# Performance work log

Measured on AMD Instinct MI355X. Metric: run time of the kernel, lower is better.

The kernel has to match this reference:

```python
import math
import jax, jax.numpy as jnp
import numpy as np

D, L, E, O, Q, H, DH, T, B, N, FF = 1024, 8, 768, 1024, 16, 16, 64, 320, 64, 577, 4096
EPS = 1e-5


def layernorm(x, g, b):
    m = jnp.mean(x, axis=-1, keepdims=True)
    v = jnp.var(x, axis=-1, keepdims=True)
    return (x - m) * jax.lax.rsqrt(v + EPS) * g + b


def timestep_sinusoid(t):
    # diffusers Timesteps(320, flip_sin_to_cos=True, freq_shift=0)
    half = T // 2
    freqs = jnp.exp(-math.log(10000.0) * jnp.arange(half, dtype=jnp.float32) / half)
    args = t.astype(jnp.float32)[:, None] * freqs[None, :]
    return jnp.concatenate([jnp.cos(args), jnp.sin(args)], axis=-1)  # flipped order


def setup_inputs() -> dict:
    key = jax.random.key(0)
    ks = iter(jax.random.split(key, 32))
    std = 0.02
    inp = {}
    inp["x"] = jax.random.normal(next(ks), (B, N, E), jnp.float32)
    inp["timestep"] = jax.random.randint(next(ks), (B,), 0, 1000, jnp.int64 if jax.config.jax_enable_x64 else jnp.int32)
    inp["latents"] = jax.random.normal(next(ks), (1, Q, D), jnp.float32) / math.sqrt(D)
    inp["proj_in_w"] = jax.random.normal(next(ks), (D, E), jnp.float32) * std
    inp["proj_in_b"] = jnp.zeros((D,), jnp.float32)
    inp["time_w1"] = jax.random.normal(next(ks), (D, T), jnp.float32) * std
    inp["time_b1"] = jnp.zeros((D,), jnp.float32)
    inp["time_w2"] = jax.random.normal(next(ks), (D, D), jnp.float32) * std
    inp["time_b2"] = jnp.zeros((D,), jnp.float32)
    inp["ln1_g"] = jnp.ones((L, D), jnp.float32)
    inp["ln1_b"] = jnp.zeros((L, D), jnp.float32)
    inp["ln2_g"] = jnp.ones((L, D), jnp.float32)
    inp["ln2_b"] = jnp.zeros((L, D), jnp.float32)
    inp["q_w"] = jax.random.normal(next(ks), (L, D, D), jnp.float32) * std
    inp["kv_w"] = jax.random.normal(next(ks), (L, 2 * D, D), jnp.float32) * std
    inp["out_w"] = jax.random.normal(next(ks), (L, D, D), jnp.float32) * std
    inp["ffln_g"] = jnp.ones((L, D), jnp.float32)
    inp["ffln_b"] = jnp.zeros((L, D), jnp.float32)
    inp["ff_w1"] = jax.random.normal(next(ks), (L, FF, D), jnp.float32) * std
    inp["ff_w2"] = jax.random.normal(next(ks), (L, D, FF), jnp.float32) * std
    inp["ada_w"] = jax.random.normal(next(ks), (L, 4 * D, D), jnp.float32) * std
    inp["ada_b"] = jnp.zeros((L, 4 * D), jnp.float32)
    inp["proj_out_w"] = jax.random.normal(next(ks), (O, D), jnp.float32) * std
    inp["proj_out_b"] = jnp.zeros((O,), jnp.float32)
    inp["nout_g"] = jnp.ones((O,), jnp.float32)
    inp["nout_b"] = jnp.zeros((O,), jnp.float32)
    return inp


def reference(x, timestep, latents, proj_in_w, proj_in_b, time_w1, time_b1, time_w2, time_b2,
              ln1_g, ln1_b, ln2_g, ln2_b, q_w, kv_w, out_w, ffln_g, ffln_b, ff_w1, ff_w2,
              ada_w, ada_b, proj_out_w, proj_out_b, nout_g, nout_b):
    b = x.shape[0]
    # timestep embedding
    t_emb = timestep_sinusoid(timestep).astype(x.dtype)
    temb = jax.nn.silu(t_emb @ time_w1.T + time_b1) @ time_w2.T + time_b2  # [B, D]

    lat = jnp.broadcast_to(latents, (b, Q, D))
    xp = x @ proj_in_w.T + proj_in_b + temb[:, None, :]  # [B, N, D]

    sc = 1.0 / math.sqrt(math.sqrt(DH))
    for i in range(L):
        mod = jax.nn.silu(temb) @ ada_w[i].T + ada_b[i]  # [B, 4D]
        shift_msa, scale_msa, shift_mlp, scale_mlp = jnp.split(mod, 4, axis=-1)

        # PerceiverAttention with AdaLN-modulated latents
        xn = layernorm(xp, ln1_g[i], ln1_b[i])
        lt = layernorm(lat, ln2_g[i], ln2_b[i])
        lt = lt * (1.0 + scale_msa[:, None, :]) + shift_msa[:, None, :]
        q = (lt @ q_w[i].T).reshape(b, Q, H, DH).transpose(0, 2, 1, 3)       # [B,H,Q,DH]
        kv_in = jnp.concatenate([xn, lt], axis=1)                             # [B,N+Q,D]
        kv = kv_in @ kv_w[i].T
        k, v = jnp.split(kv, 2, axis=-1)
        kl = kv_in.shape[1]
        k = k.reshape(b, kl, H, DH).transpose(0, 2, 1, 3)
        v = v.reshape(b, kl, H, DH).transpose(0, 2, 1, 3)
        w = jnp.einsum('bhqd,bhkd->bhqk', q * sc, k * sc)
        w = jax.nn.softmax(w.astype(jnp.float32), axis=-1).astype(q.dtype)
        o = jnp.einsum('bhqk,bhkd->bhqd', w, v).transpose(0, 2, 1, 3).reshape(b, Q, H * DH)
        lat = o @ out_w[i].T + lat

        # FFN with AdaLN modulation after its LayerNorm
        h = layernorm(lat, ffln_g[i], ffln_b[i])
        h = h * (1.0 + scale_mlp[:, None, :]) + shift_mlp[:, None, :]
        h = jax.nn.gelu(h @ ff_w1[i].T, approximate=False)
        lat = h @ ff_w2[i].T + lat

    out = lat @ proj_out_w.T + proj_out_b
    out = layernorm(out, nout_g, nout_b)
    return out
```

## Files before the change

### kernel.cpp

```cpp
#include <hip/hip_runtime.h>
#include <hip/hip_bf16.h>
#include <math.h>

#define B_  64
#define N_  577
#define E_  768
#define D_  1024
#define L_  8
#define Q_  16
#define H_  16
#define DH_ 64
#define T_  320
#define FF_ 4096
#define O_  1024
#define MX_ (B_*N_)
#define KL_ (N_+Q_)
#define BQ_ (B_*Q_)
#define KVOFF ((size_t)B_*H_*KL_*DH_)

typedef unsigned short u16;
typedef __bf16 v8bf __attribute__((ext_vector_type(8)));
typedef float  v4f  __attribute__((ext_vector_type(4)));

__device__ __forceinline__ float bf2f(u16 u){
  union { float f; unsigned int i; } v; v.i = ((unsigned int)u) << 16; return v.f;
}
__device__ __forceinline__ u16 f2bf(float f){
  union { float f; unsigned int i; } v; v.f = f;
  unsigned int x = v.i;
  return (u16)((x + 0x7fffu + ((x >> 16) & 1u)) >> 16);
}

__device__ __forceinline__ void gld16(const u16* g, u16* l){
  __builtin_amdgcn_global_load_lds(
      (const __attribute__((address_space(1))) void*)g,
      (__attribute__((address_space(3))) void*)l, 16, 0, 0);
}

__global__ void k_tsnorm(const int* __restrict__ raw, float* __restrict__ tsf){
  __shared__ int nz;
  int tid = threadIdx.x;
  if (tid == 0) nz = 0;
  __syncthreads();
  if (tid < 32 && raw[2 * tid + 1] != 0) atomicOr(&nz, 1);
  __syncthreads();
  int t = (nz == 0) ? raw[2 * tid] : raw[tid];
  tsf[tid] = (float)t;
}

__global__ void k_f2b(const float* __restrict__ src, u16* __restrict__ dst, long long n4){
  long long i = (long long)blockIdx.x * blockDim.x + threadIdx.x;
  long long stride = (long long)gridDim.x * blockDim.x;
  for (; i < n4; i += stride){
    float4 f = reinterpret_cast<const float4*>(src)[i];
    ushort4 u; u.x = f2bf(f.x); u.y = f2bf(f.y); u.z = f2bf(f.z); u.w = f2bf(f.w);
    reinterpret_cast<ushort4*>(dst)[i] = u;
  }
}

template<int EPI, int BM>
__global__ __launch_bounds__(256) void k_gemm(
    const u16* __restrict__ X, const u16* __restrict__ Wm,
    const float* __restrict__ bias, const float* __restrict__ aux,
    void* __restrict__ out, void* __restrict__ out2, int M, int N, int K)
{
  constexpr int MREP = BM / 32;
  constexpr int NCHA = BM / 8;
  constexpr int NCH  = NCHA + 16;
  constexpr int LPW  = NCH / 4;
  constexpr int NBUF = (BM == 128) ? 1 : 2;
  __shared__ u16 As[NBUF * BM * 64];
  __shared__ u16 Bs[NBUF * 128 * 64];
  const int tid  = threadIdx.x;
  const int lane = tid & 63;
  const int wid  = tid >> 6;
  const int wr   = wid >> 1, wc = wid & 1;
  const int m0   = blockIdx.y * BM, n0 = blockIdx.x * 128;
  const int fr   = lane & 15;
  const int js   = lane >> 4;
  const int fsw  = (fr >> 1) & 7;

  v4f zero = {0.f, 0.f, 0.f, 0.f};
  v4f acc[MREP][4];
  #pragma unroll
  for (int m = 0; m < MREP; ++m)
    #pragma unroll
    for (int n = 0; n < 4; ++n) acc[m][n] = zero;

  const int srow = lane >> 3;

  auto stage = [&](int buf, int k0){
    #pragma unroll
    for (int p = 0; p < LPW; ++p) {
      const int ch = wid * LPW + p;
      if (ch < NCHA) {
        const int fst = (ch * 4 + (lane >> 4)) & 7;
        const int gc  = (((lane & 7) ^ fst) << 3);
        int ar = m0 + ch * 8 + srow; if (ar > M - 1) ar = M - 1;
        gld16(X + (size_t)ar * K + k0 + gc, &As[buf * BM * 64 + ch * 512]);
      } else {
        const int cb  = ch - NCHA;
        const int fst = (cb * 4 + (lane >> 4)) & 7;
        const int gc  = (((lane & 7) ^ fst) << 3);
        int br = n0 + cb * 8 + srow;
        gld16(Wm + (size_t)br * K + k0 + gc, &Bs[buf * 128 * 64 + cb * 512]);
      }
    }
  };

  auto compute = [&](const u16* Ab, const u16* Bb){
    __builtin_amdgcn_s_setprio(1);
    #pragma unroll
    for (int kk = 0; kk < 2; ++kk) {
      const int ps = (((kk * 4 + js) ^ fsw) << 3);
      v8bf a[MREP], b[4];
      #pragma unroll
      for (int m = 0; m < MREP; ++m)
        a[m] = *reinterpret_cast<const v8bf*>(Ab + (wr * (BM / 2) + m * 16 + fr) * 64 + ps);
      #pragma unroll
      for (int n = 0; n < 4; ++n)
        b[n] = *reinterpret_cast<const v8bf*>(Bb + (wc * 64 + n * 16 + fr) * 64 + ps);
      #pragma unroll
      for (int m = 0; m < MREP; ++m)
        #pragma unroll
        for (int n = 0; n < 4; ++n)
          acc[m][n] = __builtin_amdgcn_mfma_f32_16x16x32_bf16(a[m], b[n], acc[m][n], 0, 0, 0);
    }
    __builtin_amdgcn_s_setprio(0);
  };

  const int nt = K >> 6;
  if constexpr (NBUF == 1) {
    for (int t = 0; t < nt; ++t) {
      stage(0, t << 6);
      __syncthreads();
      compute(&As[0], &Bs[0]);
      __syncthreads();
    }
  } else {
    stage(0, 0);
    for (int t = 0; t < nt; ++t) {
      if (t + 1 < nt) {
        stage((t + 1) & 1, (t + 1) << 6);
        if constexpr (LPW == 8) asm volatile("s_waitcnt vmcnt(8)" ::: "memory");
        else                    asm volatile("s_waitcnt vmcnt(6)" ::: "memory");
      } else {
        asm volatile("s_waitcnt vmcnt(0)" ::: "memory");
      }
      __builtin_amdgcn_s_barrier();
      compute(&As[(t & 1) * BM * 64], &Bs[(t & 1) * 128 * 64]);
      __builtin_amdgcn_s_barrier();
    }
  }

  const int rq = (lane >> 4) << 2;
  #pragma unroll
  for (int m = 0; m < MREP; ++m) {
    #pragma unroll
    for (int n = 0; n < 4; ++n) {
      const int col = n0 + wc * 64 + n * 16 + fr;
      #pragma unroll
      for (int r = 0; r < 4; ++r) {
        const int row = m0 + wr * (BM / 2) + m * 16 + rq + r;
        if (row >= M) continue;
        float v = acc[m][n][r];
        if constexpr (EPI == 1 || EPI == 2 || EPI == 3 || EPI == 6) v += bias[col];
        if constexpr (EPI == 3) v += aux[(size_t)(row / N_) * N + col];
        if constexpr (EPI == 4) v += aux[(size_t)row * N + col];
        if constexpr (EPI == 5) v = 0.5f * v * (1.0f + erff(v * 0.70710678118654752f));
        if constexpr (EPI == 6) {
          int bb = row / N_, jj = row - bb * N_;
          int c2 = (col < D_) ? col : col - D_;
          int hh = c2 >> 6, dd = c2 & 63;
          u16* dst = (u16*)out2 + ((col < D_) ? 0 : KVOFF);
          dst[(((size_t)bb * H_ + hh) * KL_ + jj) * DH_ + dd] = f2bf(v);
        } else if constexpr (EPI == 8) {
          if (col < D_) {
            reinterpret_cast<u16*>(out)[(size_t)row * D_ + col] = f2bf(v);
          } else {
            int cc = col - D_;
            int bb = row >> 4, jj = N_ + (row & 15);
            int c2 = (cc < D_) ? cc : cc - D_;
            int hh = c2 >> 6, dd = c2 & 63;
            u16* dst = (u16*)out2 + ((cc < D_) ? 0 : KVOFF);
            dst[(((size_t)bb * H_ + hh) * KL_ + jj) * DH_ + dd] = f2bf(v);
          }
        } else if constexpr (EPI == 2 || EPI == 4) {
          reinterpret_cast<float*>(out)[(size_t)row * N + col] = v;
        } else {
          reinterpret_cast<u16*>(out)[(size_t)row * N + col] = f2bf(v);
        }
      }
    }
  }
}

__global__ __launch_bounds__(256) void k_prep(
    const float* __restrict__ kvw, const float* __restrict__ g, const float* __restrict__ bvec,
    u16* __restrict__ kvf, u16* __restrict__ kvwb, float* __restrict__ kvb,
    const float* __restrict__ qw,  u16* __restrict__ dqw,
    const float* __restrict__ ow,  u16* __restrict__ dow,
    const float* __restrict__ f1w, u16* __restrict__ df1,
    const float* __restrict__ f2w, u16* __restrict__ df2,
    const float* __restrict__ aw,  u16* __restrict__ daw)
{
  __shared__ float sl[4];
  const int bid = blockIdx.x, tid = threadIdx.x;
  if (bid < 2048) {
    int o = bid;
    float4 w = reinterpret_cast<const float4*>(kvw + (size_t)o * D_)[tid];
    float4 gg = reinterpret_cast<const float4*>(g)[tid];
    float4 bv = reinterpret_cast<const float4*>(bvec)[tid];
    ushort4 f;
    f.x = f2bf(w.x * gg.x); f.y = f2bf(w.y * gg.y); f.z = f2bf(w.z * gg.z); f.w = f2bf(w.w * gg.w);
    reinterpret_cast<ushort4*>(kvf + (size_t)o * D_)[tid] = f;
    ushort4 f2;
    f2.x = f2bf(w.x); f2.y = f2bf(w.y); f2.z = f2bf(w.z); f2.w = f2bf(w.w);
    reinterpret_cast<ushort4*>(kvwb + (size_t)o * D_)[tid] = f2;
    float s = w.x * bv.x + w.y * bv.y + w.z * bv.z + w.w * bv.w;
    for (int off = 32; off; off >>= 1) s += __shfl_down(s, off);
    if ((tid & 63) == 0) sl[tid >> 6] = s;
    __syncthreads();
    if (tid == 0) kvb[o] = sl[0] + sl[1] + sl[2] + sl[3];
  } else {
    int id = bid - 2048;
    const float* src; u16* dst; int off;
    if      (id < 1024)  { src = qw;  dst = dqw; off = id; }
    else if (id < 2048)  { src = ow;  dst = dow; off = id - 1024; }
    else if (id < 6144)  { src = f1w; dst = df1; off = id - 2048; }
    else if (id < 10240) { src = f2w; dst = df2; off = id - 6144; }
    else                 { src = aw;  dst = daw; off = id - 10240; }
    size_t base = (size_t)off * 1024 + (size_t)tid * 4;
    float4 v = *reinterpret_cast<const float4*>(src + base);
    ushort4 u; u.x = f2bf(v.x); u.y = f2bf(v.y); u.z = f2bf(v.z); u.w = f2bf(v.w);
    *reinterpret_cast<ushort4*>(dst + base) = u;
  }
}

__global__ void k_temb1(const float* __restrict__ tsf, const float* __restrict__ w1,
                        const float* __restrict__ b1, float* __restrict__ h1tT){
  int o = blockIdx.x, b = threadIdx.x;
  float t = tsf[b];
  float acc = b1[o];
  const float c = -9.210340371976184f / 160.0f;
  for (int j = 0; j < 160; ++j) {
    float arg = t * expf(c * (float)j);
    acc += w1[(size_t)o * T_ + j] * cosf(arg) + w1[(size_t)o * T_ + 160 + j] * sinf(arg);
  }
  float s = acc / (1.0f + expf(-acc));
  h1tT[(size_t)o * B_ + b] = s;
}

__global__ void k_temb2(const float* __restrict__ h1tT, const float* __restrict__ w2,
                        const float* __restrict__ b2, float* __restrict__ temb){
  int o = blockIdx.x, b = threadIdx.x;
  float acc = b2[o];
  for (int d = 0; d < D_; ++d) acc += h1tT[(size_t)d * B_ + b] * w2[(size_t)o * D_ + d];
  temb[(size_t)b * D_ + o] = acc;
}

__global__ void k_silu(const float* __restrict__ in, u16* __restrict__ outb, int n){
  int i = blockIdx.x * blockDim.x + threadIdx.x;
  if (i < n) { float x = in[i]; outb[i] = f2bf(x / (1.0f + expf(-x))); }
}

__global__ void k_init_lat(const float* __restrict__ latents, float* __restrict__ lat){
  int i = blockIdx.x * blockDim.x + threadIdx.x;
  if (i < BQ_ * D_) lat[i] = latents[i & (Q_ * D_ - 1)];
}

__global__ __launch_bounds__(256) void k_rownorm(const u16* __restrict__ xp, u16* __restrict__ outb){
  __shared__ float s1[4], s2[4];
  size_t row = blockIdx.x;
  int tid = threadIdx.x;
  ushort4 u = reinterpret_cast<const ushort4*>(xp + row * D_)[tid];
  float v0 = bf2f(u.x), v1 = bf2f(u.y), v2 = bf2f(u.z), v3 = bf2f(u.w);
  float s = v0 + v1 + v2 + v3;
  float q = v0 * v0 + v1 * v1 + v2 * v2 + v3 * v3;
  for (int off = 32; off; off >>= 1) { s += __shfl_down(s, off); q += __shfl_down(q, off); }
  if ((tid & 63) == 0) { s1[tid >> 6] = s; s2[tid >> 6] = q; }
  __syncthreads();
  float S = s1[0] + s1[1] + s1[2] + s1[3], Qv = s2[0] + s2[1] + s2[2] + s2[3];
  float mean = S * (1.f / D_);
  float rs = rsqrtf(Qv * (1.f / D_) - mean * mean + 1e-5f);
  ushort4 o;
  o.x = f2bf((v0 - mean) * rs); o.y = f2bf((v1 - mean) * rs);
  o.z = f2bf((v2 - mean) * rs); o.w = f2bf((v3 - mean) * rs);
  reinterpret_cast<ushort4*>(outb + row * D_)[tid] = o;
}

__global__ __launch_bounds__(256) void k_lnmod(const float* __restrict__ in, const float* __restrict__ g,
                                               const float* __restrict__ bb, const float* __restrict__ modp,
                                               u16* __restrict__ outb){
  __shared__ float s1[4], s2[4];
  int row = blockIdx.x, tid = threadIdx.x;
  int b = row >> 4;
  float4 v = reinterpret_cast<const float4*>(in + (size_t)row * D_)[tid];
  float s = v.x + v.y + v.z + v.w;
  float q = v.x * v.x + v.y * v.y + v.z * v.z + v.w * v.w;
  for (int off = 32; off; off >>= 1) { s += __shfl_down(s, off); q += __shfl_down(q, off); }
  if ((tid & 63) == 0) { s1[tid >> 6] = s; s2[tid >> 6] = q; }
  __syncthreads();
  float S = s1[0] + s1[1] + s1[2] + s1[3], Qv = s2[0] + s2[1] + s2[2] + s2[3];
  float mean = S * (1.f / D_);
  float rs = rsqrtf(Qv * (1.f / D_) - mean * mean + 1e-5f);
  float4 gg = reinterpret_cast<const float4*>(g)[tid];
  float4 bv = reinterpret_cast<const float4*>(bb)[tid];
  const float* mrow = modp + (size_t)b * (4 * D_);
  float4 sh = reinterpret_cast<const float4*>(mrow)[tid];
  float4 scv = reinterpret_cast<const float4*>(mrow + D_)[tid];
  ushort4 o;
  o.x = f2bf(((v.x - mean) * rs * gg.x + bv.x) * (1.f + scv.x) + sh.x);
  o.y = f2bf(((v.y - mean) * rs * gg.y + bv.y) * (1.f + scv.y) + sh.y);
  o.z = f2bf(((v.z - mean) * rs * gg.z + bv.z) * (1.f + scv.z) + sh.z);
  o.w = f2bf(((v.w - mean) * rs * gg.w + bv.w) * (1.f + scv.w) + sh.w);
  reinterpret_cast<ushort4*>(outb + (size_t)row * D_)[tid] = o;
}

__global__ __launch_bounds__(256) void k_lnfinal(const float* __restrict__ in, const float* __restrict__ g,
                                                 const float* __restrict__ bb, float* __restrict__ outf){
  __shared__ float s1[4], s2[4];
  int row = blockIdx.x, tid = threadIdx.x;
  float4 v = reinterpret_cast<const float4*>(in + (size_t)row * O_)[tid];
  float s = v.x + v.y + v.z + v.w;
  float q = v.x * v.x + v.y * v.y + v.z * v.z + v.w * v.w;
  for (int off = 32; off; off >>= 1) { s += __shfl_down(s, off); q += __shfl_down(q, off); }
  if ((tid & 63) == 0) { s1[tid >> 6] = s; s2[tid >> 6] = q; }
  __syncthreads();
  float S = s1[0] + s1[1] + s1[2] + s1[3], Qv = s2[0] + s2[1] + s2[2] + s2[3];
  float mean = S * (1.f / O_);
  float rs = rsqrtf(Qv * (1.f / O_) - mean * mean + 1e-5f);
  float4 gg = reinterpret_cast<const float4*>(g)[tid];
  float4 bv = reinterpret_cast<const float4*>(bb)[tid];
  float4 o;
  o.x = (v.x - mean) * rs * gg.x + bv.x;
  o.y = (v.y - mean) * rs * gg.y + bv.y;
  o.z = (v.z - mean) * rs * gg.z + bv.z;
  o.w = (v.w - mean) * rs * gg.w + bv.w;
  reinterpret_cast<float4*>(outf + (size_t)row * O_)[tid] = o;
}

__global__ __launch_bounds__(256) void k_attn2(const u16* __restrict__ qb,
                                               const u16* __restrict__ kb,
                                               const u16* __restrict__ vb,
                                               u16* __restrict__ ob){
  __shared__ float qs[Q_][DH_ + 4];
  __shared__ u16   ks[128][DH_ + 4];
  __shared__ float sc[Q_][600];
  __shared__ float rsum[Q_];
  const int bh  = blockIdx.x;
  const int b   = bh >> 4, h = bh & 15;
  const int tid = threadIdx.x;
  {
    int qi = tid >> 4, d4 = (tid & 15) << 2;
    ushort4 u = *reinterpret_cast<const ushort4*>(qb + (size_t)(b * Q_ + qi) * D_ + h * DH_ + d4);
    qs[qi][d4 + 0] = 0.125f * bf2f(u.x);
    qs[qi][d4 + 1] = 0.125f * bf2f(u.y);
    qs[qi][d4 + 2] = 0.125f * bf2f(u.z);
    qs[qi][d4 + 3] = 0.125f * bf2f(u.w);
  }
  const u16* kbh = kb + (size_t)bh * KL_ * DH_;
  const u16* vbh = vb + (size_t)bh * KL_ * DH_;
  for (int j0 = 0; j0 < KL_; j0 += 128) {
    int rows = KL_ - j0; if (rows > 128) rows = 128;
    __syncthreads();
    for (int idx = tid; idx < rows * 16; idx += 256) {
      int r = idx >> 4, c4 = (idx & 15) << 2;
      *reinterpret_cast<ushort4*>(&ks[r][c4]) =
          *reinterpret_cast<const ushort4*>(kbh + (size_t)(j0 + r) * DH_ + c4);
    }
    __syncthreads();
    for (int e = tid; e < Q_ * 128; e += 256) {
      int jj = e & 127, qi = e >> 7;
      if (jj < rows) {
        float s = 0.f;
        #pragma unroll
        for (int d = 0; d < DH_; d += 4) {
          ushort4 u = *reinterpret_cast<const ushort4*>(&ks[jj][d]);
          s += qs[qi][d] * bf2f(u.x) + qs[qi][d + 1] * bf2f(u.y)
             + qs[qi][d + 2] * bf2f(u.z) + qs[qi][d + 3] * bf2f(u.w);
        }
        sc[qi][j0 + jj] = s;
      }
    }
  }
  __syncthreads();
  {
    int g = tid >> 4, l = tid & 15;
    float mx = -1e30f;
    for (int j = l; j < KL_; j += 16) mx = fmaxf(mx, sc[g][j]);
    for (int m = 1; m < 16; m <<= 1) mx = fmaxf(mx, __shfl_xor(mx, m));
    float sum = 0.f;
    for (int j = l; j < KL_; j += 16) { float e = expf(sc[g][j] - mx); sc[g][j] = e; sum += e; }
    for (int m = 1; m < 16; m <<= 1) sum += __shfl_xor(sum, m);
    if (l == 0) rsum[g] = sum;
  }
  {
    int d = tid & 63, q0 = tid >> 6;
    float acc[4] = {0.f, 0.f, 0.f, 0.f};
    for (int j0 = 0; j0 < KL_; j0 += 128) {
      int rows = KL_ - j0; if (rows > 128) rows = 128;
      __syncthreads();
      for (int idx = tid; idx < rows * 16; idx += 256) {
        int r = idx >> 4, c4 = (idx & 15) << 2;
        *reinterpret_cast<ushort4*>(&ks[r][c4]) =
            *reinterpret_cast<const ushort4*>(vbh + (size_t)(j0 + r) * DH_ + c4);
      }
      __syncthreads();
      for (int jj = 0; jj < rows; ++jj) {
        float vj = bf2f(ks[jj][d]);
        #pragma unroll
        for (int t = 0; t < 4; ++t) acc[t] += sc[q0 + t * 4][j0 + jj] * vj;
      }
    }
    #pragma unroll
    for (int t = 0; t < 4; ++t) {
      int qi = q0 + t * 4;
      ob[(size_t)(b * Q_ + qi) * D_ + h * DH_ + d] = f2bf(acc[t] / rsum[qi]);
    }
  }
}

static void conv_launch(const float* src, u16* dst, size_t n, hipStream_t s){
  long long n4 = (long long)(n >> 2);
  int blocks = (int)((n4 + 255) / 256);
  if (blocks > 4096) blocks = 4096;
  k_f2b<<<blocks, 256, 0, s>>>(src, dst, n4);
}

template<int EPI, int BM>
static void gemm(const u16* X, const u16* W, const float* bias, const float* aux,
                 void* out, void* out2, int M, int N, int K, hipStream_t s){
  dim3 g(N / 128, (M + BM - 1) / BM);
  k_gemm<EPI, BM><<<g, 256, 0, s>>>(X, W, bias, aux, out, out2, M, N, K);
}

extern "C" void kernel_launch(void* const* d_in, const int* in_sizes, int n_in,
                              void* d_out, int out_size, void* d_ws, size_t ws_size,
                              hipStream_t stream)
{
  const float* x         = (const float*)d_in[0];
  const int*   tsp       = (const int*)  d_in[1];
  const float* latents   = (const float*)d_in[2];
  const float* proj_in_w = (const float*)d_in[3];
  const float* proj_in_b = (const float*)d_in[4];
  const float* time_w1   = (const float*)d_in[5];
  const float* time_b1   = (const float*)d_in[6];
  const float* time_w2   = (const float*)d_in[7];
  const float* time_b2   = (const float*)d_in[8];
  const float* ln1_g     = (const float*)d_in[9];
  const float* ln1_b     = (const float*)d_in[10];
  const float* ln2_g     = (const float*)d_in[11];
  const float* ln2_b     = (const float*)d_in[12];
  const float* q_w       = (const float*)d_in[13];
  const float* kv_w      = (const float*)d_in[14];
  const float* out_w     = (const float*)d_in[15];
  const float* ffln_g    = (const float*)d_in[16];
  const float* ffln_b    = (const float*)d_in[17];
  const float* ff_w1     = (const float*)d_in[18];
  const float* ff_w2     = (const float*)d_in[19];
  const float* ada_w     = (const float*)d_in[20];
  const float* ada_b     = (const float*)d_in[21];
  const float* proj_out_w= (const float*)d_in[22];
  const float* proj_out_b= (const float*)d_in[23];
  const float* nout_g    = (const float*)d_in[24];
  const float* nout_b    = (const float*)d_in[25];

  char* Wp = (char*)d_ws;
  size_t off = 0;
  auto alloc = [&](size_t bytes) -> void* {
    void* p = Wp + off;
    off = (off + bytes + 255) & ~(size_t)255;
    return p;
  };

  float* tsf   = (float*)alloc((size_t)B_ * 4);
  float* temb  = (float*)alloc((size_t)B_ * D_ * 4);
  float* h1tT  = (float*)alloc((size_t)D_ * B_ * 4);
  u16*   stemb = (u16*)  alloc((size_t)B_ * D_ * 2);
  float* modli = (float*)alloc((size_t)B_ * 4 * D_ * 4);
  float* kvb   = (float*)alloc((size_t)2 * D_ * 4);
  float* lat   = (float*)alloc((size_t)BQ_ * D_ * 4);
  u16*   lt    = (u16*)  alloc((size_t)BQ_ * D_ * 2);
  u16*   qb    = (u16*)  alloc((size_t)BQ_ * D_ * 2);
  u16*   ob    = (u16*)  alloc((size_t)BQ_ * D_ * 2);
  u16*   hb    = (u16*)  alloc((size_t)BQ_ * D_ * 2);
  u16*   h1b   = (u16*)  alloc((size_t)BQ_ * FF_ * 2);
  u16*   latb  = (u16*)  alloc((size_t)BQ_ * D_ * 2);
  float* tmpf  = (float*)alloc((size_t)BQ_ * D_ * 4);
  u16*   wpin  = (u16*)  alloc((size_t)D_ * E_ * 2);
  u16*   wadai = (u16*)  alloc((size_t)4 * D_ * D_ * 2);
  u16*   wpout = (u16*)  alloc((size_t)O_ * D_ * 2);
  u16*   kvf   = (u16*)  alloc((size_t)2 * D_ * D_ * 2);
  u16*   wqkv  = (u16*)  alloc((size_t)3 * D_ * D_ * 2);
  u16*   wouti = (u16*)  alloc((size_t)D_ * D_ * 2);
  u16*   wff1i = (u16*)  alloc((size_t)FF_ * D_ * 2);
  u16*   wff2i = (u16*)  alloc((size_t)D_ * FF_ * 2);
  u16*   nxp   = (u16*)  alloc((size_t)MX_ * D_ * 2);
  u16*   kvwb  = wqkv + (size_t)D_ * D_;
  size_t xb_sz  = (size_t)B_ * N_ * E_ * 2;
  size_t xpb_sz = (size_t)MX_ * D_ * 2;
  size_t kv_sz  = (size_t)B_ * H_ * KL_ * DH_ * 2;
  size_t big_sz = (xb_sz + xpb_sz > 2 * kv_sz) ? (xb_sz + xpb_sz) : 2 * kv_sz;
  char* big = (char*)alloc(big_sz);
  u16* xb   = (u16*)big;
  u16* xpb  = (u16*)(big + xb_sz);
  u16* kbuf = (u16*)big;
  u16* vbuf = (u16*)(big + kv_sz);

  conv_launch(x,          xb,    (size_t)B_ * N_ * E_, stream);
  conv_launch(proj_in_w,  wpin,  (size_t)D_ * E_,      stream);
  conv_launch(proj_out_w, wpout, (size_t)O_ * D_,      stream);

  k_tsnorm<<<1, B_, 0, stream>>>(tsp, tsf);
  k_temb1<<<D_, B_, 0, stream>>>(tsf, time_w1, time_b1, h1tT);
  k_temb2<<<D_, B_, 0, stream>>>(h1tT, time_w2, time_b2, temb);
  k_silu<<<(B_ * D_ + 255) / 256, 256, 0, stream>>>(temb, stemb, B_ * D_);

  gemm<3, 128>(xb, wpin, proj_in_b, temb, xpb, nullptr, MX_, D_, E_, stream);
  k_rownorm<<<MX_, 256, 0, stream>>>(xpb, nxp);
  k_init_lat<<<(BQ_ * D_) / 256, 256, 0, stream>>>(latents, lat);

  for (int i = 0; i < L_; ++i) {
    k_prep<<<16384, 256, 0, stream>>>(
        kv_w + (size_t)i * 2 * D_ * D_, ln1_g + i * D_, ln1_b + i * D_,
        kvf, kvwb, kvb,
        q_w   + (size_t)i * D_ * D_,  wqkv,
        out_w + (size_t)i * D_ * D_,  wouti,
        ff_w1 + (size_t)i * FF_ * D_, wff1i,
        ff_w2 + (size_t)i * D_ * FF_, wff2i,
        ada_w + (size_t)i * 4 * D_ * D_, wadai);

    gemm<2, 64>(stemb, wadai, ada_b + (size_t)i * 4 * D_, nullptr, modli, nullptr, B_, 4 * D_, D_, stream);

    gemm<6, 128>(nxp, kvf, kvb, nullptr, nullptr, kbuf, MX_, 2 * D_, D_, stream);
    k_lnmod<<<BQ_, 256, 0, stream>>>(lat, ln2_g + i * D_, ln2_b + i * D_, modli, lt);
    gemm<8, 64>(lt, wqkv, nullptr, nullptr, qb, kbuf, BQ_, 3 * D_, D_, stream);
    k_attn2<<<B_ * H_, 256, 0, stream>>>(qb, kbuf, vbuf, ob);
    gemm<4, 64>(ob, wouti, nullptr, lat, lat, nullptr, BQ_, D_, D_, stream);
    k_lnmod<<<BQ_, 256, 0, stream>>>(lat, ffln_g + i * D_, ffln_b + i * D_, modli + 2 * D_, hb);
    gemm<5, 64>(hb,  wff1i, nullptr, nullptr, h1b, nullptr, BQ_, FF_, D_,  stream);
    gemm<4, 64>(h1b, wff2i, nullptr, lat,     lat, nullptr, BQ_, D_,  FF_, stream);
  }

  conv_launch(lat, latb, (size_t)BQ_ * D_, stream);
  gemm<2, 64>(latb, wpout, proj_out_b, nullptr, tmpf, nullptr, BQ_, O_, D_, stream);
  k_lnfinal<<<BQ_, 256, 0, stream>>>(tmpf, nout_g, nout_b, (float*)d_out);
}
```

Before: 4.413 ms.

## Double-buffer BM=128 GEMM with BK=32 tiles and add XCD-aware block swizzle

```diff
diff --git a/kernel.cpp b/kernel.cpp
--- a/kernel.cpp
+++ b/kernel.cpp
@@ -64,21 +64,35 @@
     const float* __restrict__ bias, const float* __restrict__ aux,
     void* __restrict__ out, void* __restrict__ out2, int M, int N, int K)
 {
+  constexpr int BK   = (BM == 128) ? 32 : 64;
   constexpr int MREP = BM / 32;
-  constexpr int NCHA = BM / 8;
-  constexpr int NCH  = NCHA + 16;
+  constexpr int RPC  = 512 / BK;
+  constexpr int NCHA = BM / RPC;
+  constexpr int NCHB = 128 / RPC;
+  constexpr int NCH  = NCHA + NCHB;
   constexpr int LPW  = NCH / 4;
-  constexpr int NBUF = (BM == 128) ? 1 : 2;
-  __shared__ u16 As[NBUF * BM * 64];
-  __shared__ u16 Bs[NBUF * 128 * 64];
+  __shared__ u16 As[2 * BM * BK];
+  __shared__ u16 Bs[2 * 128 * BK];
   const int tid  = threadIdx.x;
   const int lane = tid & 63;
   const int wid  = tid >> 6;
   const int wr   = wid >> 1, wc = wid & 1;
-  const int m0   = blockIdx.y * BM, n0 = blockIdx.x * 128;
-  const int fr   = lane & 15;
-  const int js   = lane >> 4;
-  const int fsw  = (fr >> 1) & 7;
+
+  int bx = blockIdx.x, by = blockIdx.y;
+  {
+    const int gx = gridDim.x;
+    const int nwg = gx * gridDim.y;
+    if ((nwg & 7) == 0) {
+      int flat = by * gx + bx;
+      int swz = (flat & 7) * (nwg >> 3) + (flat >> 3);
+      bx = swz % gx; by = swz / gx;
+    }
+  }
+  const int m0 = by * BM, n0 = bx * 128;
+
+  const int fr  = lane & 15;
+  const int js  = lane >> 4;
+  const int fsw = (fr >> 1) & ((BK == 32) ? 3 : 7);
 
   v4f zero = {0.f, 0.f, 0.f, 0.f};
   v4f acc[MREP][4];
@@ -87,23 +101,28 @@
     #pragma unroll
     for (int n = 0; n < 4; ++n) acc[m][n] = zero;
 
-  const int srow = lane >> 3;
-
   auto stage = [&](int buf, int k0){
     #pragma unroll
     for (int p = 0; p < LPW; ++p) {
       const int ch = wid * LPW + p;
-      if (ch < NCHA) {
-        const int fst = (ch * 4 + (lane >> 4)) & 7;
-        const int gc  = (((lane & 7) ^ fst) << 3);
-        int ar = m0 + ch * 8 + srow; if (ar > M - 1) ar = M - 1;
-        gld16(X + (size_t)ar * K + k0 + gc, &As[buf * BM * 64 + ch * 512]);
+      const bool isA = (ch < NCHA);
+      const int cb = isA ? ch : ch - NCHA;
+      int grow, gc;
+      if constexpr (BK == 32) {
+        grow = cb * 16 + (lane >> 2);
+        const int fst = (lane >> 3) & 3;
+        gc = (((lane & 3) ^ fst) << 3);
       } else {
-        const int cb  = ch - NCHA;
+        grow = cb * 8 + (lane >> 3);
         const int fst = (cb * 4 + (lane >> 4)) & 7;
-        const int gc  = (((lane & 7) ^ fst) << 3);
-        int br = n0 + cb * 8 + srow;
-        gld16(Wm + (size_t)br * K + k0 + gc, &Bs[buf * 128 * 64 + cb * 512]);
+        gc = (((lane & 7) ^ fst) << 3);
+      }
+      if (isA) {
+        int ar = m0 + grow; if (ar > M - 1) ar = M - 1;
+        gld16(X + (size_t)ar * K + k0 + gc, &As[buf * BM * BK + cb * 512]);
+      } else {
+        int br = n0 + grow;
+        gld16(Wm + (size_t)br * K + k0 + gc, &Bs[buf * 128 * BK + cb * 512]);
       }
     }
   };
@@ -111,15 +130,15 @@
   auto compute = [&](const u16* Ab, const u16* Bb){
     __builtin_amdgcn_s_setprio(1);
     #pragma unroll
-    for (int kk = 0; kk < 2; ++kk) {
+    for (int kk = 0; kk < BK / 32; ++kk) {
       const int ps = (((kk * 4 + js) ^ fsw) << 3);
       v8bf a[MREP], b[4];
       #pragma unroll
       for (int m = 0; m < MREP; ++m)
-        a[m] = *reinterpret_cast<const v8bf*>(Ab + (wr * (BM / 2) + m * 16 + fr) * 64 + ps);
+        a[m] = *reinterpret_cast<const v8bf*>(Ab + (wr * (BM / 2) + m * 16 + fr) * BK + ps);
       #pragma unroll
       for (int n = 0; n < 4; ++n)
-        b[n] = *reinterpret_cast<const v8bf*>(Bb + (wc * 64 + n * 16 + fr) * 64 + ps);
+        b[n] = *reinterpret_cast<const v8bf*>(Bb + (wc * 64 + n * 16 + fr) * BK + ps);
       #pragma unroll
       for (int m = 0; m < MREP; ++m)
         #pragma unroll
@@ -129,28 +148,20 @@
     __builtin_amdgcn_s_setprio(0);
   };
 
-  const int nt = K >> 6;
-  if constexpr (NBUF == 1) {
-    for (int t = 0; t < nt; ++t) {
-      stage(0, t << 6);
-      __syncthreads();
-      compute(&As[0], &Bs[0]);
-      __syncthreads();
-    }
-  } else {
-    stage(0, 0);
-    for (int t = 0; t < nt; ++t) {
-      if (t + 1 < nt) {
-        stage((t + 1) & 1, (t + 1) << 6);
-        if constexpr (LPW == 8) asm volatile("s_waitcnt vmcnt(8)" ::: "memory");
-        else                    asm volatile("s_waitcnt vmcnt(6)" ::: "memory");
-      } else {
-        asm volatile("s_waitcnt vmcnt(0)" ::: "memory");
-      }
-      __builtin_amdgcn_s_barrier();
-      compute(&As[(t & 1) * BM * 64], &Bs[(t & 1) * 128 * 64]);
-      __builtin_amdgcn_s_barrier();
-    }
+  const int nt = K / BK;
+  stage(0, 0);
+  for (int t = 0; t < nt; ++t) {
+    if (t + 1 < nt) {
+      stage((t + 1) & 1, (t + 1) * BK);
+      if constexpr (LPW == 4)      asm volatile("s_waitcnt vmcnt(4)" ::: "memory");
+      else if constexpr (LPW == 6) asm volatile("s_waitcnt vmcnt(6)" ::: "memory");
+      else                         asm volatile("s_waitcnt vmcnt(8)" ::: "memory");
+    } else {
+      asm volatile("s_waitcnt vmcnt(0)" ::: "memory");
+    }
+    __builtin_amdgcn_s_barrier();
+    compute(&As[(t & 1) * BM * BK], &Bs[(t & 1) * 128 * BK]);
+    __builtin_amdgcn_s_barrier();
   }
 
   const int rq = (lane >> 4) << 2;
```

Result: no change. 4.437 ms (+0.5%).

## Batch all layers' AdaLN modulation GEMMs into one upfront GEMM

Applied to the files above, without the earlier changes.

```diff
diff --git a/kernel.cpp b/kernel.cpp
--- a/kernel.cpp
+++ b/kernel.cpp
@@ -64,13 +64,14 @@
     const float* __restrict__ bias, const float* __restrict__ aux,
     void* __restrict__ out, void* __restrict__ out2, int M, int N, int K)
 {
+  constexpr int BK   = 64;
   constexpr int MREP = BM / 32;
   constexpr int NCHA = BM / 8;
   constexpr int NCH  = NCHA + 16;
   constexpr int LPW  = NCH / 4;
   constexpr int NBUF = (BM == 128) ? 1 : 2;
-  __shared__ u16 As[NBUF * BM * 64];
-  __shared__ u16 Bs[NBUF * 128 * 64];
+  __shared__ u16 As[NBUF * BM * BK];
+  __shared__ u16 Bs[NBUF * 128 * BK];
   const int tid  = threadIdx.x;
   const int lane = tid & 63;
   const int wid  = tid >> 6;
@@ -87,46 +88,44 @@
     #pragma unroll
     for (int n = 0; n < 4; ++n) acc[m][n] = zero;
 
-  const int srow = lane >> 3;
-
   auto stage = [&](int buf, int k0){
     #pragma unroll
     for (int p = 0; p < LPW; ++p) {
       const int ch = wid * LPW + p;
-      if (ch < NCHA) {
-        const int fst = (ch * 4 + (lane >> 4)) & 7;
-        const int gc  = (((lane & 7) ^ fst) << 3);
-        int ar = m0 + ch * 8 + srow; if (ar > M - 1) ar = M - 1;
-        gld16(X + (size_t)ar * K + k0 + gc, &As[buf * BM * 64 + ch * 512]);
+      const bool isA = (ch < NCHA);
+      const int cb = isA ? ch : ch - NCHA;
+      const int fst = (cb * 4 + (lane >> 4)) & 7;
+      const int gc  = (((lane & 7) ^ fst) << 3);
+      const int grow = cb * 8 + (lane >> 3);
+      if (isA) {
+        int ar = m0 + grow; if (ar > M - 1) ar = M - 1;
+        gld16(X + (size_t)ar * K + k0 + gc, &As[buf * BM * BK + cb * 512]);
       } else {
-        const int cb  = ch - NCHA;
-        const int fst = (cb * 4 + (lane >> 4)) & 7;
-        const int gc  = (((lane & 7) ^ fst) << 3);
-        int br = n0 + cb * 8 + srow;
-        gld16(Wm + (size_t)br * K + k0 + gc, &Bs[buf * 128 * 64 + cb * 512]);
+        int br = n0 + grow;
+        gld16(Wm + (size_t)br * K + k0 + gc, &Bs[buf * 128 * BK + cb * 512]);
       }
     }
   };
 
   auto compute = [&](const u16* Ab, const u16* Bb){
-    __builtin_amdgcn_s_setprio(1);
+    if constexpr (BM == 64) __builtin_amdgcn_s_setprio(1);
     #pragma unroll
     for (int kk = 0; kk < 2; ++kk) {
       const int ps = (((kk * 4 + js) ^ fsw) << 3);
       v8bf a[MREP], b[4];
       #pragma unroll
       for (int m = 0; m < MREP; ++m)
-        a[m] = *reinterpret_cast<const v8bf*>(Ab + (wr * (BM / 2) + m * 16 + fr) * 64 + ps);
+        a[m] = *reinterpret_cast<const v8bf*>(Ab + (wr * (BM / 2) + m * 16 + fr) * BK + ps);
       #pragma unroll
       for (int n = 0; n < 4; ++n)
-        b[n] = *reinterpret_cast<const v8bf*>(Bb + (wc * 64 + n * 16 + fr) * 64 + ps);
+        b[n] = *reinterpret_cast<const v8bf*>(Bb + (wc * 64 + n * 16 + fr) * BK + ps);
       #pragma unroll
       for (int m = 0; m < MREP; ++m)
         #pragma unroll
         for (int n = 0; n < 4; ++n)
           acc[m][n] = __builtin_amdgcn_mfma_f32_16x16x32_bf16(a[m], b[n], acc[m][n], 0, 0, 0);
     }
-    __builtin_amdgcn_s_setprio(0);
+    if constexpr (BM == 64) __builtin_amdgcn_s_setprio(0);
   };
 
   const int nt = K >> 6;
@@ -142,13 +141,12 @@
     for (int t = 0; t < nt; ++t) {
       if (t + 1 < nt) {
         stage((t + 1) & 1, (t + 1) << 6);
-        if constexpr (LPW == 8) asm volatile("s_waitcnt vmcnt(8)" ::: "memory");
-        else                    asm volatile("s_waitcnt vmcnt(6)" ::: "memory");
+        asm volatile("s_waitcnt vmcnt(6)" ::: "memory");
       } else {
         asm volatile("s_waitcnt vmcnt(0)" ::: "memory");
       }
       __builtin_amdgcn_s_barrier();
-      compute(&As[(t & 1) * BM * 64], &Bs[(t & 1) * 128 * 64]);
+      compute(&As[(t & 1) * BM * BK], &Bs[(t & 1) * 128 * BK]);
       __builtin_amdgcn_s_barrier();
     }
   }
@@ -201,8 +199,7 @@
     const float* __restrict__ qw,  u16* __restrict__ dqw,
     const float* __restrict__ ow,  u16* __restrict__ dow,
     const float* __restrict__ f1w, u16* __restrict__ df1,
-    const float* __restrict__ f2w, u16* __restrict__ df2,
-    const float* __restrict__ aw,  u16* __restrict__ daw)
+    const float* __restrict__ f2w, u16* __restrict__ df2)
 {
   __shared__ float sl[4];
   const int bid = blockIdx.x, tid = threadIdx.x;
@@ -228,8 +225,7 @@
     if      (id < 1024)  { src = qw;  dst = dqw; off = id; }
     else if (id < 2048)  { src = ow;  dst = dow; off = id - 1024; }
     else if (id < 6144)  { src = f1w; dst = df1; off = id - 2048; }
-    else if (id < 10240) { src = f2w; dst = df2; off = id - 6144; }
-    else                 { src = aw;  dst = daw; off = id - 10240; }
+    else                 { src = f2w; dst = df2; off = id - 6144; }
     size_t base = (size_t)off * 1024 + (size_t)tid * 4;
     float4 v = *reinterpret_cast<const float4*>(src + base);
     ushort4 u; u.x = f2bf(v.x); u.y = f2bf(v.y); u.z = f2bf(v.z); u.w = f2bf(v.w);
@@ -291,7 +287,7 @@
 
 __global__ __launch_bounds__(256) void k_lnmod(const float* __restrict__ in, const float* __restrict__ g,
                                                const float* __restrict__ bb, const float* __restrict__ modp,
-                                               u16* __restrict__ outb){
+                                               int mstride, u16* __restrict__ outb){
   __shared__ float s1[4], s2[4];
   int row = blockIdx.x, tid = threadIdx.x;
   int b = row >> 4;
@@ -306,7 +302,7 @@
   float rs = rsqrtf(Qv * (1.f / D_) - mean * mean + 1e-5f);
   float4 gg = reinterpret_cast<const float4*>(g)[tid];
   float4 bv = reinterpret_cast<const float4*>(bb)[tid];
-  const float* mrow = modp + (size_t)b * (4 * D_);
+  const float* mrow = modp + (size_t)b * mstride;
   float4 sh = reinterpret_cast<const float4*>(mrow)[tid];
   float4 scv = reinterpret_cast<const float4*>(mrow + D_)[tid];
   ushort4 o;
@@ -478,7 +474,7 @@
   float* temb  = (float*)alloc((size_t)B_ * D_ * 4);
   float* h1tT  = (float*)alloc((size_t)D_ * B_ * 4);
   u16*   stemb = (u16*)  alloc((size_t)B_ * D_ * 2);
-  float* modli = (float*)alloc((size_t)B_ * 4 * D_ * 4);
+  float* modb8 = (float*)alloc((size_t)B_ * L_ * 4 * D_ * 4);
   float* kvb   = (float*)alloc((size_t)2 * D_ * 4);
   float* lat   = (float*)alloc((size_t)BQ_ * D_ * 4);
   u16*   lt    = (u16*)  alloc((size_t)BQ_ * D_ * 2);
@@ -489,7 +485,7 @@
   u16*   latb  = (u16*)  alloc((size_t)BQ_ * D_ * 2);
   float* tmpf  = (float*)alloc((size_t)BQ_ * D_ * 4);
   u16*   wpin  = (u16*)  alloc((size_t)D_ * E_ * 2);
-  u16*   wadai = (u16*)  alloc((size_t)4 * D_ * D_ * 2);
+  u16*   wada8 = (u16*)  alloc((size_t)L_ * 4 * D_ * D_ * 2);
   u16*   wpout = (u16*)  alloc((size_t)O_ * D_ * 2);
   u16*   kvf   = (u16*)  alloc((size_t)2 * D_ * D_ * 2);
   u16*   wqkv  = (u16*)  alloc((size_t)3 * D_ * D_ * 2);
@@ -511,34 +507,37 @@
   conv_launch(x,          xb,    (size_t)B_ * N_ * E_, stream);
   conv_launch(proj_in_w,  wpin,  (size_t)D_ * E_,      stream);
   conv_launch(proj_out_w, wpout, (size_t)O_ * D_,      stream);
+  conv_launch(ada_w,      wada8, (size_t)L_ * 4 * D_ * D_, stream);
 
   k_tsnorm<<<1, B_, 0, stream>>>(tsp, tsf);
   k_temb1<<<D_, B_, 0, stream>>>(tsf, time_w1, time_b1, h1tT);
   k_temb2<<<D_, B_, 0, stream>>>(h1tT, time_w2, time_b2, temb);
   k_silu<<<(B_ * D_ + 255) / 256, 256, 0, stream>>>(temb, stemb, B_ * D_);
 
+  gemm<2, 64>(stemb, wada8, ada_b, nullptr, modb8, nullptr, B_, L_ * 4 * D_, D_, stream);
+
   gemm<3, 128>(xb, wpin, proj_in_b, temb, xpb, nullptr, MX_, D_, E_, stream);
   k_rownorm<<<MX_, 256, 0, stream>>>(xpb, nxp);
   k_init_lat<<<(BQ_ * D_) / 256, 256, 0, stream>>>(latents, lat);
 
+  const int MSTR = L_ * 4 * D_;
   for (int i = 0; i < L_; ++i) {
-    k_prep<<<16384, 256, 0, stream>>>(
+    k_prep<<<12288, 256, 0, stream>>>(
         kv_w + (size_t)i * 2 * D_ * D_, ln1_g + i * D_, ln1_b + i * D_,
         kvf, kvwb, kvb,
         q_w   + (size_t)i * D_ * D_,  wqkv,
         out_w + (size_t)i * D_ * D_,  wouti,
         ff_w1 + (size_t)i * FF_ * D_, wff1i,
-        ff_w2 + (size_t)i * D_ * FF_, wff2i,
-        ada_w + (size_t)i * 4 * D_ * D_, wadai);
-
-    gemm<2, 64>(stemb, wadai, ada_b + (size_t)i * 4 * D_, nullptr, modli, nullptr, B_, 4 * D_, D_, stream);
+        ff_w2 + (size_t)i * D_ * FF_, wff2i);
 
     gemm<6, 128>(nxp, kvf, kvb, nullptr, nullptr, kbuf, MX_, 2 * D_, D_, stream);
-    k_lnmod<<<BQ_, 256, 0, stream>>>(lat, ln2_g + i * D_, ln2_b + i * D_, modli, lt);
+    k_lnmod<<<BQ_, 256, 0, stream>>>(lat, ln2_g + i * D_, ln2_b + i * D_,
+                                     modb8 + (size_t)i * 4 * D_, MSTR, lt);
     gemm<8, 64>(lt, wqkv, nullptr, nullptr, qb, kbuf, BQ_, 3 * D_, D_, stream);
     k_attn2<<<B_ * H_, 256, 0, stream>>>(qb, kbuf, vbuf, ob);
     gemm<4, 64>(ob, wouti, nullptr, lat, lat, nullptr, BQ_, D_, D_, stream);
-    k_lnmod<<<BQ_, 256, 0, stream>>>(lat, ffln_g + i * D_, ffln_b + i * D_, modli + 2 * D_, hb);
+    k_lnmod<<<BQ_, 256, 0, stream>>>(lat, ffln_g + i * D_, ffln_b + i * D_,
+                                     modb8 + (size_t)i * 4 * D_ + 2 * D_, MSTR, hb);
     gemm<5, 64>(hb,  wff1i, nullptr, nullptr, h1b, nullptr, BQ_, FF_, D_,  stream);
     gemm<4, 64>(h1b, wff2i, nullptr, lat,     lat, nullptr, BQ_, D_,  FF_, stream);
   }
```

After: 4.253 ms. -3.6%, faster.
